# Optimization experiments

Measured on AMD Instinct MI355X. Metric: run time of the kernel, lower is better.

## Reference

```python
import jax, jax.numpy as jnp
import numpy as np
import math

D_MODEL = 256; N_LEVELS = 5; N_HEADS = 8; N_POINTS = 4
D_HEAD = D_MODEL // N_HEADS
BS = 1; T = 5; H = 64; W = 96


def conv3x3(x, w, b):
    # x: (N, C, H, W), w: (O, C, 3, 3) -> SAME padding conv
    y = jax.lax.conv_general_dilated(x, w, (1, 1), ((1, 1), (1, 1)),
                                     dimension_numbers=('NCHW', 'OIHW', 'NCHW'))
    return y + b[None, :, None, None]


def bilinear_zero(img, px, py):
    # img: (C, Hh, Ww); px, py: (...) pixel coords; zero padding outside.
    C, Hh, Ww = img.shape
    x0 = jnp.floor(px); y0 = jnp.floor(py)
    wx1 = px - x0; wx0 = 1.0 - wx1
    wy1 = py - y0; wy0 = 1.0 - wy1

    def gather(xi, yi):
        valid = (xi >= 0) & (xi < Ww) & (yi >= 0) & (yi < Hh)
        xc = jnp.clip(xi, 0, Ww - 1).astype(jnp.int32)
        yc = jnp.clip(yi, 0, Hh - 1).astype(jnp.int32)
        return img[:, yc, xc] * valid.astype(img.dtype)

    return (gather(x0, y0) * (wx0 * wy0) + gather(x0 + 1, y0) * (wx1 * wy0)
            + gather(x0, y0 + 1) * (wx0 * wy1) + gather(x0 + 1, y0 + 1) * (wx1 * wy1))


def warp(x, flo):
    # x: (b, c, h, w), flo: (b, 2, h, w); grid_sample(align_corners=True) equivalent
    b, c, h, w = x.shape
    gy, gx = jnp.meshgrid(jnp.arange(h, dtype=x.dtype), jnp.arange(w, dtype=x.dtype), indexing='ij')
    px = gx[None] + flo[:, 0]
    py = gy[None] + flo[:, 1]
    return jax.vmap(bilinear_zero)(x, px, py)


def flow_guid_offset(ff, fb, offset):
    # ff, fb: (b, 4, 2, h, w); offset: (N, T*h*w, heads, L, P, 2)
    N, THW, heads, L, P, _ = offset.shape
    hw = THW // L
    off = offset.reshape(N, L, hw, heads, L, P, 2)
    f01, f12, f23, f34 = ff[:, 0], ff[:, 1], ff[:, 2], ff[:, 3]
    f02 = f01 + warp(f12, f01)
    f03 = f02 + warp(f23, f02)
    f04 = f03 + warp(f34, f03)
    f13 = f12 + warp(f23, f12)
    f14 = f13 + warp(f34, f13)
    f24 = f23 + warp(f34, f23)
    b10, b21, b32, b43 = fb[:, 0], fb[:, 1], fb[:, 2], fb[:, 3]
    b42 = b43 + warp(b32, b43)
    b41 = b42 + warp(b21, b42)
    b40 = b41 + warp(b10, b41)
    b31 = b32 + warp(b21, b32)
    b30 = b31 + warp(b10, b31)
    b20 = b21 + warp(b10, b21)

    def flat(f):  # (b, 2, h, w) -> (b, hw, 2)
        return f.transpose(0, 2, 3, 1).reshape(f.shape[0], -1, 2)

    z = jnp.zeros_like(flat(f01))
    adds = jnp.stack([
        jnp.stack([z, flat(f01), flat(f02), flat(f03), flat(f04)], axis=2),
        jnp.stack([flat(b10), z, flat(f12), flat(f13), flat(f14)], axis=2),
        jnp.stack([flat(b20), flat(b21), z, flat(f23), flat(f24)], axis=2),
        jnp.stack([flat(b30), flat(b31), flat(b32), z, flat(f34)], axis=2),
        # NOTE: source repeats chunk3's flows for chunk4 (kept faithfully)
        jnp.stack([flat(b30), flat(b31), flat(b32), z, flat(f34)], axis=2),
    ], axis=1)  # (b, L, hw, L, 2)
    off = off + adds[:, :, :, None, :, None, :]
    return off.reshape(N, THW, heads, L, P, 2)


def _forward(query, input_flatten, reference_points, input_spatial_shapes,
             input_level_start_index, input_padding_mask, flow_forward, flow_backward,
             w_off, b_off, w_attn, b_attn, w_val, b_val, w_out, b_out):
    bs, t, c, h, w = query.shape
    q2 = query.reshape(bs * t, c, h, w)
    value = conv3x3(input_flatten.reshape(bs * t, c, h, w), w_val, b_val)
    off = conv3x3(q2, w_off, b_off)      # (bs*t, heads*L*P*2, h, w)
    aw = conv3x3(q2, w_attn, b_attn)     # (bs*t, heads*L*P, h, w)
    Lq = t * h * w

    def to_tokens(x):  # (bs*t, C, h, w) -> (bs, t*h*w, C)
        return x.reshape(bs, t, -1, h * w).transpose(0, 1, 3, 2).reshape(bs, Lq, -1)

    value = to_tokens(value)
    off = to_tokens(off)
    aw = to_tokens(aw)
    value = jnp.where(input_padding_mask[..., None], jnp.zeros((), value.dtype), value)
    value = value.reshape(bs, Lq, N_HEADS, D_HEAD)
    off = off.reshape(bs, Lq, N_HEADS, N_LEVELS, N_POINTS, 2)
    off = flow_guid_offset(flow_forward, flow_backward, off)
    aw = jax.nn.softmax(aw.reshape(bs, Lq, N_HEADS, N_LEVELS * N_POINTS), axis=-1)
    aw = aw.reshape(bs, Lq, N_HEADS, N_LEVELS, N_POINTS)
    # sampling locations, normalized by (W_l, H_l)
    normalizer = jnp.stack([input_spatial_shapes[:, 1], input_spatial_shapes[:, 0]], -1).astype(off.dtype)
    loc = reference_points[:, :, None, :, None, :] + off / normalizer[None, None, None, :, None, :]
    # core: multi-scale deformable bilinear sampling (grid_sample align_corners=False)
    value_lvl = value.reshape(bs, t, h * w, N_HEADS, D_HEAD)
    out = jnp.zeros((bs * N_HEADS, D_HEAD, Lq), dtype=value.dtype)
    for lvl in range(N_LEVELS):
        v = value_lvl[:, lvl].reshape(bs, h, w, N_HEADS, D_HEAD)
        v = v.transpose(0, 3, 4, 1, 2).reshape(bs * N_HEADS, D_HEAD, h, w)
        l = loc[:, :, :, lvl]  # (bs, Lq, heads, P, 2)
        px = (l[..., 0] * w - 0.5).transpose(0, 2, 1, 3).reshape(bs * N_HEADS, Lq, N_POINTS)
        py = (l[..., 1] * h - 0.5).transpose(0, 2, 1, 3).reshape(bs * N_HEADS, Lq, N_POINTS)
        samp = jax.vmap(bilinear_zero)(v, px, py)  # (bs*heads, D_HEAD, Lq, P)
        w_l = aw[:, :, :, lvl].transpose(0, 2, 1, 3).reshape(bs * N_HEADS, 1, Lq, N_POINTS)
        out = out + jnp.sum(samp * w_l, axis=-1)
    out = out.reshape(bs, N_HEADS, D_HEAD, Lq).transpose(0, 3, 1, 2).reshape(bs, Lq, c)
    out = out.reshape(bs, t, h * w, c).transpose(0, 1, 3, 2).reshape(bs * t, c, h, w)
    out = conv3x3(out, w_out, b_out)
    return out.reshape(bs, t, c, h, w)


def setup_inputs() -> dict:
    key = jax.random.key(0)
    ks = jax.random.split(key, 10)
    Lq = T * H * W
    query = jax.random.normal(ks[0], (BS, T, D_MODEL, H, W), jnp.float32)
    input_flatten = jax.random.normal(ks[1], (BS, T, D_MODEL, H, W), jnp.float32)
    reference_points = jax.random.uniform(ks[2], (BS, Lq, N_LEVELS, 2), jnp.float32)
    input_spatial_shapes = jnp.tile(jnp.array([[H, W]], jnp.int32), (N_LEVELS, 1))
    input_level_start_index = jnp.arange(N_LEVELS, dtype=jnp.int32) * (H * W)
    input_padding_mask = jnp.zeros((BS, Lq), dtype=bool)
    flow_forward = jax.random.normal(ks[3], (BS, 4, 2, H, W), jnp.float32) * 2.0
    flow_backward = jax.random.normal(ks[4], (BS, 4, 2, H, W), jnp.float32) * 2.0

    def xavier(k, shape):
        fan_in = shape[1] * shape[2] * shape[3]
        fan_out = shape[0] * shape[2] * shape[3]
        lim = math.sqrt(6.0 / (fan_in + fan_out))
        return jax.random.uniform(k, shape, jnp.float32, -lim, lim)

    w_off = jax.random.normal(ks[5], (N_HEADS * N_LEVELS * N_POINTS * 2, D_MODEL, 3, 3), jnp.float32) * 0.01
    # bias init follows _reset_parameters grid_init
    thetas = np.arange(N_HEADS) * (2.0 * np.pi / N_HEADS)
    grid = np.stack([np.cos(thetas), np.sin(thetas)], -1)
    grid = grid / np.abs(grid).max(-1, keepdims=True)
    grid = np.tile(grid.reshape(N_HEADS, 1, 1, 2), (1, N_LEVELS, N_POINTS, 1))
    for i in range(N_POINTS):
        grid[:, :, i, :] *= i + 1
    b_off = jnp.asarray(grid.reshape(-1), jnp.float32)
    w_attn = jax.random.normal(ks[6], (N_HEADS * N_LEVELS * N_POINTS, D_MODEL, 3, 3), jnp.float32) * 0.01
    b_attn = jnp.zeros((N_HEADS * N_LEVELS * N_POINTS,), jnp.float32)
    w_val = xavier(ks[7], (D_MODEL, D_MODEL, 3, 3)); b_val = jnp.zeros((D_MODEL,), jnp.float32)
    w_out = xavier(ks[8], (D_MODEL, D_MODEL, 3, 3)); b_out = jnp.zeros((D_MODEL,), jnp.float32)
    return {"query": query, "input_flatten": input_flatten, "reference_points": reference_points,
            "input_spatial_shapes": input_spatial_shapes, "input_level_start_index": input_level_start_index,
            "input_padding_mask": input_padding_mask, "flow_forward": flow_forward, "flow_backward": flow_backward,
            "w_off": w_off, "b_off": b_off, "w_attn": w_attn, "b_attn": b_attn,
            "w_val": w_val, "b_val": b_val, "w_out": w_out, "b_out": b_out}


def reference(query, input_flatten, reference_points, input_spatial_shapes,
              input_level_start_index, input_padding_mask, flow_forward, flow_backward,
              w_off, b_off, w_attn, b_attn, w_val, b_val, w_out, b_out):
    return _forward(query, input_flatten, reference_points, input_spatial_shapes,
                    input_level_start_index, input_padding_mask, flow_forward, flow_backward,
                    w_off, b_off, w_attn, b_attn, w_val, b_val, w_out, b_out)
```

## Files before the change

### kernel.cpp

```cpp
#include <hip/hip_runtime.h>
#include <hip/hip_bf16.h>
#include <hip/hip_fp16.h>

typedef __hip_bfloat16 bf16;
typedef __attribute__((ext_vector_type(8))) short short8;
typedef __attribute__((ext_vector_type(4))) float float4v;

#define T_  5
#define H_  64
#define W_  96
#define HW_ (H_*W_)
#define C_  256
#define NH_ 8
#define DH_ 32
#define NL_ 5
#define NP_ 4
#define LQ_ (T_*HW_)
#define UNITS_ (LQ_*NH_)

#define PH_ 66
#define PW_ 98

static __device__ __forceinline__ void gl2lds16(const bf16* g, bf16* l){
  __builtin_amdgcn_global_load_lds(
      (const __attribute__((address_space(1))) unsigned int*)g,
      (__attribute__((address_space(3))) unsigned int*)l, 16, 0, 0);
}

__global__ __launch_bounds__(256) void zfill_k(float4* __restrict__ p, int n4){
  int i = blockIdx.x*256 + threadIdx.x;
  if (i < n4){ float4 z; z.x=z.y=z.z=z.w=0.f; p[i]=z; }
}

__global__ __launch_bounds__(256) void pad_in_k(const float* __restrict__ in0,
                                                const float* __restrict__ in1,
                                                bf16* __restrict__ pad0,
                                                bf16* __restrict__ pad1){
  __shared__ bf16 sb[256][66];
  const float* in = blockIdx.z ? in1 : in0;
  bf16* pad       = blockIdx.z ? pad1 : pad0;
  int t = blockIdx.y;
  int pix0 = blockIdx.x*64;
  int tid = threadIdx.x;
  int pl = tid & 63, cg = tid >> 6;
  #pragma unroll 4
  for (int it=0; it<64; ++it){
    int c = it*4 + cg;
    sb[c][pl] = __float2bfloat16(in[((size_t)t*C_ + c)*HW_ + pix0 + pl]);
  }
  __syncthreads();
  for (int p=0; p<64; ++p){
    int pix = pix0 + p;
    int y = pix/W_, x = pix - y*W_;
    pad[(((size_t)t*PH_ + y+1)*PW_ + x+1)*C_ + tid] = sb[tid][p];
  }
}

#define S0_ 589824
#define S1_ 1179648
__global__ __launch_bounds__(256) void wt_all_k(const float* __restrict__ wv,
                                                const float* __restrict__ wo,
                                                const float* __restrict__ wa,
                                                const float* __restrict__ wout,
                                                const float* __restrict__ bo,
                                                const float* __restrict__ ba,
                                                bf16* __restrict__ WTv,
                                                bf16* __restrict__ WToa,
                                                bf16* __restrict__ WTout,
                                                float* __restrict__ boa){
  int idx = blockIdx.x*256 + threadIdx.x;
  if (idx < S0_){
    int n = idx/2304, r = idx - n*2304; int tap = r>>8, ci = r&255;
    WTv[idx] = __float2bfloat16(wv[((size_t)(n*C_+ci))*9 + tap]);
  } else if (idx < S0_+S1_){
    int k = idx - S0_;
    int n = k/2304, r = k - n*2304; int tap=r>>8, ci=r&255;
    float v = 0.f;
    if (n < 320)      v = wo[((size_t)(n*C_+ci))*9+tap];
    else if (n < 480) v = wa[((size_t)((n-320)*C_+ci))*9+tap];
    WToa[k] = __float2bfloat16(v);
  } else if (idx < S0_+S1_+S0_){
    int k = idx - S0_ - S1_;
    int n = k/2304, r = k - n*2304; int tap=r>>8, ci=r&255;
    WTout[k] = __float2bfloat16(wout[((size_t)(n*C_+ci))*9+tap]);
  } else if (idx < S0_+S1_+S0_+512){
    int n = idx - (S0_+S1_+S0_);
    float v = 0.f;
    if (n < 320) v = bo[n]; else if (n < 480) v = ba[n-320];
    boa[n] = v;
  }
}

#define BM 128
#define BN 256
#define BK 64

__global__ __launch_bounds__(256,2) void gemm12_k(const bf16* __restrict__ Av,
                                                  const bf16* __restrict__ Aq,
                                                  const bf16* __restrict__ WTv,
                                                  const bf16* __restrict__ WToa,
                                                  const float* __restrict__ bv,
                                                  const float* __restrict__ boa,
                                                  bf16* __restrict__ outv,
                                                  float* __restrict__ P,
                                                  float* __restrict__ aw){
  __shared__ __align__(16) bf16 As[BM*BK];
  __shared__ __align__(16) bf16 Bs[BN*BK];
  int tid = threadIdx.x;
  int lane = tid & 63, wvi = tid >> 6;
  int wm = wvi & 1, wn = wvi >> 1;
  int quad = lane >> 4, l15 = lane & 15;
  int bx = blockIdx.x, byy = blockIdx.y;
  bool isval = byy == 0;
  const bf16* Apad  = isval ? Av  : Aq;
  const bf16* WT    = isval ? WTv : WToa;
  const float* bias = isval ? bv  : boa;
  int nby = isval ? 0 : byy - 1;

  int srow = tid >> 3;
  int c8   = (tid & 7) ^ (srow & 7);
  long abase[4];
  #pragma unroll
  for (int j=0;j<4;++j){
    int p = j*32 + srow;
    int Pm = bx*BM + p;
    int t = Pm / HW_, rem = Pm - t*HW_;
    int y = rem / W_, x = rem - y*W_;
    abase[j] = ((long)(t*PH_ + y)*PW_ + x)*C_ + c8*8;
  }
  const bf16* bbase = WT + (size_t)(nby*BN + srow)*2304 + c8*8;

  float4v acc[4][8];
  #pragma unroll
  for (int jn=0;jn<8;++jn){
    float bvv = bias[nby*BN + wn*128 + jn*16 + l15];
    #pragma unroll
    for (int i=0;i<4;++i){ acc[i][jn][0]=bvv; acc[i][jn][1]=bvv; acc[i][jn][2]=bvv; acc[i][jn][3]=bvv; }
  }

  for (int kt=0; kt<36; ++kt){
    int tap = kt >> 2, kc = (kt & 3) << 6;
    int dy = tap/3, dx = tap - dy*3;
    long ash = (long)(dy*PW_ + dx)*C_ + kc;
    long bsh = (long)kt*64;
    __syncthreads();
    #pragma unroll
    for (int j=0;j<4;++j)
      gl2lds16(Apad + abase[j] + ash, As + (j*256+tid)*8);
    #pragma unroll
    for (int j=0;j<8;++j)
      gl2lds16(bbase + (size_t)j*32*2304 + bsh, Bs + (j*256+tid)*8);
    __syncthreads();
    #pragma unroll
    for (int kk=0; kk<2; ++kk){
      int slot = ((kk<<2) + quad) ^ (l15 & 7);
      short8 af[4], bfr[8];
      #pragma unroll
      for (int jn=0;jn<8;++jn)
        bfr[jn] = *(const short8*)(Bs + (wn*128 + jn*16 + l15)*BK + slot*8);
      #pragma unroll
      for (int i=0;i<4;++i)
        af[i] = *(const short8*)(As + (wm*64 + i*16 + l15)*BK + slot*8);
      #pragma unroll
      for (int i=0;i<4;++i)
        #pragma unroll
        for (int jn=0;jn<8;++jn)
          acc[i][jn] = __builtin_amdgcn_mfma_f32_16x16x32_bf16(af[i], bfr[jn], acc[i][jn], 0,0,0);
    }
  }

  #pragma unroll
  for (int i=0;i<4;++i){
    int mr = bx*BM + wm*64 + i*16 + quad*4;
    #pragma unroll
    for (int jn=0;jn<8;++jn){
      int nc = nby*BN + wn*128 + jn*16 + l15;
      #pragma unroll
      for (int r=0;r<4;++r){
        float v = acc[i][jn][r];
        long m = mr + r;
        if (isval){
          outv[m*256 + nc] = __float2bfloat16(v);
        } else {
          if (nc < 320){
            int h = nc/40, rr = nc - h*40;
            int l = rr >> 3, pxy = rr & 7;
            P[((size_t)l*UNITS_ + m*8 + h)*8 + pxy] = v;
          } else if (nc < 480){
            int hh = (nc-320)/20, ii = (nc-320) - hh*20;
            aw[((size_t)m*8 + hh)*20 + ii] = v;
          }
        }
      }
    }
  }
}

__global__ __launch_bounds__(256,2) void gemm_out_k(const bf16* __restrict__ Apad,
                                                    const bf16* __restrict__ WT,
                                                    const float* __restrict__ bias,
                                                    float* __restrict__ out){
  __shared__ __align__(16) bf16 As[BM*BK];
  __shared__ __align__(16) bf16 Bs[BN*BK];
  int tid = threadIdx.x;
  int lane = tid & 63, wvi = tid >> 6;
  int wm = wvi & 1, wn = wvi >> 1;
  int quad = lane >> 4, l15 = lane & 15;
  int bx = blockIdx.x;

  int srow = tid >> 3;
  int c8   = (tid & 7) ^ (srow & 7);
  long abase[4];
  #pragma unroll
  for (int j=0;j<4;++j){
    int p = j*32 + srow;
    int Pm = bx*BM + p;
    int t = Pm / HW_, rem = Pm - t*HW_;
    int y = rem / W_, x = rem - y*W_;
    abase[j] = ((long)(t*PH_ + y)*PW_ + x)*C_ + c8*8;
  }
  const bf16* bbase = WT + (size_t)srow*2304 + c8*8;

  float4v acc[4][8];
  #pragma unroll
  for (int jn=0;jn<8;++jn){
    float bvv = bias[wn*128 + jn*16 + l15];
    #pragma unroll
    for (int i=0;i<4;++i){ acc[i][jn][0]=bvv; acc[i][jn][1]=bvv; acc[i][jn][2]=bvv; acc[i][jn][3]=bvv; }
  }

  for (int kt=0; kt<36; ++kt){
    int tap = kt >> 2, kc = (kt & 3) << 6;
    int dy = tap/3, dx = tap - dy*3;
    long ash = (long)(dy*PW_ + dx)*C_ + kc;
    long bsh = (long)kt*64;
    __syncthreads();
    #pragma unroll
    for (int j=0;j<4;++j)
      gl2lds16(Apad + abase[j] + ash, As + (j*256+tid)*8);
    #pragma unroll
    for (int j=0;j<8;++j)
      gl2lds16(bbase + (size_t)j*32*2304 + bsh, Bs + (j*256+tid)*8);
    __syncthreads();
    #pragma unroll
    for (int kk=0; kk<2; ++kk){
      int slot = ((kk<<2) + quad) ^ (l15 & 7);
      short8 af[4], bfr[8];
      #pragma unroll
      for (int jn=0;jn<8;++jn)
        bfr[jn] = *(const short8*)(Bs + (wn*128 + jn*16 + l15)*BK + slot*8);
      #pragma unroll
      for (int i=0;i<4;++i)
        af[i] = *(const short8*)(As + (wm*64 + i*16 + l15)*BK + slot*8);
      #pragma unroll
      for (int i=0;i<4;++i)
        #pragma unroll
        for (int jn=0;jn<8;++jn)
          acc[i][jn] = __builtin_amdgcn_mfma_f32_16x16x32_bf16(af[i], bfr[jn], acc[i][jn], 0,0,0);
    }
  }

  int t = (bx*BM) / HW_;
  #pragma unroll
  for (int i=0;i<4;++i){
    int m = bx*BM + wm*64 + i*16 + quad*4;
    int pix = m - t*HW_;
    #pragma unroll
    for (int jn=0;jn<8;++jn){
      int nc = wn*128 + jn*16 + l15;
      *(float4v*)(out + ((size_t)(t*C_ + nc))*HW_ + pix) = acc[i][jn];
    }
  }
}

static __device__ __forceinline__ float bilin2(const float* __restrict__ img,
                                               float px, float py){
  float x0f = floorf(px), y0f = floorf(py);
  int x0 = (int)x0f, y0 = (int)y0f;
  float fx = px - x0f, fy = py - y0f;
  int x1 = x0+1, y1 = y0+1;
  bool vx0 = (x0>=0)&&(x0<W_), vx1 = (x1>=0)&&(x1<W_);
  bool vy0 = (y0>=0)&&(y0<H_), vy1 = (y1>=0)&&(y1<H_);
  float c00 = (vx0&&vy0)? img[y0*W_+x0] : 0.f;
  float c10 = (vx1&&vy0)? img[y0*W_+x1] : 0.f;
  float c01 = (vx0&&vy1)? img[y1*W_+x0] : 0.f;
  float c11 = (vx1&&vy1)? img[y1*W_+x1] : 0.f;
  return c00*(1.f-fx)*(1.f-fy) + c10*fx*(1.f-fy) + c01*(1.f-fx)*fy + c11*fx*fy;
}

__global__ __launch_bounds__(256) void flow_init_k(const float* __restrict__ ff,
                                                   const float* __restrict__ fb,
                                                   float* __restrict__ flows){
  int i = blockIdx.x*256 + threadIdx.x;
  const int per = 2*HW_;
  if (i >= 7*per) return;
  int f = i/per, r = i - f*per;
  float v; int slot;
  if (f < 4) { v = ff[f*per + r]; slot = f; }
  else       { v = fb[(f-4)*per + r]; slot = 10+(f-4); }
  flows[slot*per + r] = v;
}

struct Comps { int dst[5]; int a[5]; int src[5]; };

__global__ __launch_bounds__(256) void flow_compose_k(float* __restrict__ flows, Comps c){
  int ci  = blockIdx.y;
  int pix = blockIdx.x*256 + threadIdx.x;
  float* D       = flows + c.dst[ci]*2*HW_;
  const float* A = flows + c.a[ci]  *2*HW_;
  const float* S = flows + c.src[ci]*2*HW_;
  float ax = A[pix], ay = A[HW_+pix];
  float px = (float)(pix % W_) + ax;
  float py = (float)(pix / W_) + ay;
  D[pix]      = ax + bilin2(S,      px, py);
  D[HW_+pix]  = ay + bilin2(S+HW_,  px, py);
}

__device__ const int g_slotTab[25] = {
  -1,  0,  4,  5,  6,
  10, -1,  1,  7,  8,
  13, 11, -1,  2,  9,
  15, 14, 12, -1,  3,
  15, 14, 12, -1,  3 };

__global__ __launch_bounds__(256) void prep_k(const float* __restrict__ aw,
                                              const float* __restrict__ ref,
                                              const float* __restrict__ flows,
                                              float* __restrict__ P,
                                              __half* __restrict__ w16){
  int unit = blockIdx.x*256 + threadIdx.x;
  const float4* p4 = (const float4*)(aw + (size_t)unit*20);
  float4 v[5];
  #pragma unroll
  for (int i=0;i<5;++i) v[i] = p4[i];
  float* e = (float*)v;
  float m = -1e30f;
  #pragma unroll
  for (int i=0;i<20;++i) m = fmaxf(m, e[i]);
  float s = 0.f;
  #pragma unroll
  for (int i=0;i<20;++i){ e[i] = __expf(e[i]-m); s += e[i]; }
  float inv = 1.f/s;
  __half2* o2 = (__half2*)(w16 + (size_t)unit*20);
  #pragma unroll
  for (int i=0;i<10;++i)
    o2[i] = __floats2half2_rn(e[2*i]*inv, e[2*i+1]*inv);

  int q = unit >> 3;
  int t_q = q / HW_, pix = q - t_q*HW_;
  #pragma unroll
  for (int l=0; l<NL_; ++l){
    int slot = g_slotTab[t_q*5+l];
    float ax=0.f, ay=0.f;
    if (slot >= 0){ ax = flows[slot*2*HW_ + pix]; ay = flows[slot*2*HW_ + HW_ + pix]; }
    float bx = ref[(q*5+l)*2+0]*(float)W_ - 0.5f + ax;
    float by = ref[(q*5+l)*2+1]*(float)H_ - 0.5f + ay;
    float2* pp = (float2*)(P + ((size_t)l*UNITS_ + unit)*8);
    #pragma unroll
    for (int p=0;p<4;++p){ float2 t = pp[p]; t.x += bx; t.y += by; pp[p] = t; }
  }
}

template<bool FIRST, bool LAST>
__global__ __launch_bounds__(256) void phase_k(const unsigned* __restrict__ vimg0,
                                               const float2*  __restrict__ Pl,
                                               const __half*  __restrict__ wl,
                                               __half2* __restrict__ acc,
                                               bf16* __restrict__ attn_pad){
  __shared__ float4 sW[16][4];
  __shared__ int4   sI[16][4];
  int tid = threadIdx.x;
  if (tid < 64){
    int g = tid >> 2, p = tid & 3;
    int unit = blockIdx.x*16 + g;
    float2 pp = Pl[(size_t)unit*4 + p];
    float w = __half2float(wl[(size_t)unit*20 + p]);
    float x0f = floorf(pp.x), y0f = floorf(pp.y);
    float fx = pp.x - x0f,    fy = pp.y - y0f;
    int x0 = (int)x0f, y0 = (int)y0f;
    int x1 = x0+1, y1 = y0+1;
    float wx0 = 1.f-fx, wx1 = fx, wy0 = 1.f-fy, wy1 = fy;
    if ((unsigned)x0 >= (unsigned)W_) wx0 = 0.f;
    if ((unsigned)x1 >= (unsigned)W_) wx1 = 0.f;
    if ((unsigned)y0 >= (unsigned)H_) wy0 = 0.f;
    if ((unsigned)y1 >= (unsigned)H_) wy1 = 0.f;
    int xc0 = min(max(x0,0),W_-1), xc1 = min(max(x1,0),W_-1);
    int yc0 = min(max(y0,0),H_-1), yc1 = min(max(y1,0),H_-1);
    sW[g][p] = make_float4(w*wx0*wy0, w*wx1*wy0, w*wx0*wy1, w*wx1*wy1);
    sI[g][p] = make_int4((yc0*W_+xc0)*128, (yc0*W_+xc1)*128,
                         (yc1*W_+xc0)*128, (yc1*W_+xc1)*128);
  }
  __syncthreads();
  int g = tid >> 4, e = tid & 15;
  int unit = blockIdx.x*16 + g;
  int q = unit >> 3, h = unit & 7;
  const unsigned* vimg = vimg0 + h*16 + e;
  float a0, a1;
  if (FIRST){ a0 = 0.f; a1 = 0.f; }
  else { __half2 c = acc[(size_t)unit*16 + e]; a0 = __low2float(c); a1 = __high2float(c); }
  #pragma unroll
  for (int p=0; p<4; ++p){
    float4 w4 = sW[g][p];
    int4   i4 = sI[g][p];
    unsigned u00 = vimg[i4.x], u10 = vimg[i4.y];
    unsigned u01 = vimg[i4.z], u11 = vimg[i4.w];
    union {unsigned v; float f;} lo, hi;
    lo.v = u00<<16; hi.v = u00 & 0xffff0000u;
    a0 = fmaf(w4.x, lo.f, a0); a1 = fmaf(w4.x, hi.f, a1);
    lo.v = u10<<16; hi.v = u10 & 0xffff0000u;
    a0 = fmaf(w4.y, lo.f, a0); a1 = fmaf(w4.y, hi.f, a1);
    lo.v = u01<<16; hi.v = u01 & 0xffff0000u;
    a0 = fmaf(w4.z, lo.f, a0); a1 = fmaf(w4.z, hi.f, a1);
    lo.v = u11<<16; hi.v = u11 & 0xffff0000u;
    a0 = fmaf(w4.w, lo.f, a0); a1 = fmaf(w4.w, hi.f, a1);
  }
  if (LAST){
    int t_q = q / HW_, pix = q - t_q*HW_;
    int yq = pix / W_, xq = pix - yq*W_;
    union {unsigned u; bf16 hh[2];} pk;
    pk.hh[0] = __float2bfloat16(a0);
    pk.hh[1] = __float2bfloat16(a1);
    *(unsigned*)(attn_pad + (((size_t)t_q*PH_ + yq+1)*PW_ + xq+1)*C_ + h*DH_ + e*2) = pk.u;
  } else {
    acc[(size_t)unit*16 + e] = __floats2half2_rn(a0, a1);
  }
}

extern "C" void kernel_launch(void* const* d_in, const int* in_sizes, int n_in,
                              void* d_out, int out_size, void* d_ws, size_t ws_size,
                              hipStream_t stream) {
  const float* query   = (const float*)d_in[0];
  const float* in_flat = (const float*)d_in[1];
  const float* refpts  = (const float*)d_in[2];
  const float* ff      = (const float*)d_in[6];
  const float* fb      = (const float*)d_in[7];
  const float* w_off   = (const float*)d_in[8];
  const float* b_off   = (const float*)d_in[9];
  const float* w_attn  = (const float*)d_in[10];
  const float* b_attn  = (const float*)d_in[11];
  const float* w_val   = (const float*)d_in[12];
  const float* b_val   = (const float*)d_in[13];
  const float* w_out   = (const float*)d_in[14];
  const float* b_out   = (const float*)d_in[15];
  float* out = (float*)d_out;

  char* ws = (char*)d_ws;
  bf16*  v_pad   = (bf16*) (ws + 0);
  bf16*  q_pad   = (bf16*) (ws + 16558080);
  __half* w16    = (__half*)(ws + 16558080);
  bf16*  v_val   = (bf16*) (ws + 33116160);
  float* P       = (float*)(ws + 48844800);
  float* v_aw    = (float*)(ws + 88166400);
  __half2* acc   = (__half2*)(ws + 88166400);
  float* v_flows = (float*)(ws + 107827200);
  bf16*  WT_val  = (bf16*) (ws + 108613632);
  bf16*  WT_oa   = (bf16*) (ws + 109793280);
  bf16*  WT_out  = (bf16*) (ws + 112152576);
  float* bias_oa = (float*)(ws + 113332224);
  bf16*  attn_pad = v_pad;
  if (ws_size < (size_t)113334272) return;

  zfill_k<<<(2069760+255)/256, 256, 0, stream>>>((float4*)v_pad, 2069760);

  wt_all_k<<<(S0_+S1_+S0_+512+255)/256, 256, 0, stream>>>(
      w_val, w_off, w_attn, w_out, b_off, b_attn, WT_val, WT_oa, WT_out, bias_oa);

  flow_init_k<<<(7*2*HW_+255)/256, 256, 0, stream>>>(ff, fb, v_flows);
  Comps A;
  A.dst[0]=4;  A.a[0]=0;  A.src[0]=1;
  A.dst[1]=7;  A.a[1]=1;  A.src[1]=2;
  A.dst[2]=9;  A.a[2]=2;  A.src[2]=3;
  A.dst[3]=13; A.a[3]=11; A.src[3]=10;
  A.dst[4]=14; A.a[4]=12; A.src[4]=11;
  flow_compose_k<<<dim3(HW_/256,5), 256, 0, stream>>>(v_flows, A);
  Comps B;
  B.dst[0]=5;  B.a[0]=4;  B.src[0]=2;
  B.dst[1]=8;  B.a[1]=7;  B.src[1]=3;
  B.dst[2]=15; B.a[2]=14; B.src[2]=10;
  B.dst[3]=0;  B.a[3]=0;  B.src[3]=0;
  B.dst[4]=0;  B.a[4]=0;  B.src[4]=0;
  flow_compose_k<<<dim3(HW_/256,3), 256, 0, stream>>>(v_flows, B);
  Comps Cc;
  Cc.dst[0]=6; Cc.a[0]=5; Cc.src[0]=3;
  Cc.dst[1]=0; Cc.a[1]=0; Cc.src[1]=0;
  Cc.dst[2]=0; Cc.a[2]=0; Cc.src[2]=0;
  Cc.dst[3]=0; Cc.a[3]=0; Cc.src[3]=0;
  Cc.dst[4]=0; Cc.a[4]=0; Cc.src[4]=0;
  flow_compose_k<<<dim3(HW_/256,1), 256, 0, stream>>>(v_flows, Cc);

  pad_in_k<<<dim3(HW_/64, T_, 2), 256, 0, stream>>>(in_flat, query, v_pad, q_pad);

  gemm12_k<<<dim3(240, 3), 256, 0, stream>>>(v_pad, q_pad, WT_val, WT_oa,
                                             b_val, bias_oa, v_val, P, v_aw);

  prep_k<<<UNITS_/256, 256, 0, stream>>>(v_aw, refpts, v_flows, P, w16);

  {
    const unsigned* vb = (const unsigned*)v_val;
    phase_k<true ,false><<<UNITS_/16, 256, 0, stream>>>(vb + 0ul*HW_*128,
        (const float2*)(P + 0ul*UNITS_*8), w16 + 0,  acc, attn_pad);
    phase_k<false,false><<<UNITS_/16, 256, 0, stream>>>(vb + 1ul*HW_*128,
        (const float2*)(P + 1ul*UNITS_*8), w16 + 4,  acc, attn_pad);
    phase_k<false,false><<<UNITS_/16, 256, 0, stream>>>(vb + 2ul*HW_*128,
        (const float2*)(P + 2ul*UNITS_*8), w16 + 8,  acc, attn_pad);
    phase_k<false,false><<<UNITS_/16, 256, 0, stream>>>(vb + 3ul*HW_*128,
        (const float2*)(P + 3ul*UNITS_*8), w16 + 12, acc, attn_pad);
    phase_k<false,true ><<<UNITS_/16, 256, 0, stream>>>(vb + 4ul*HW_*128,
        (const float2*)(P + 4ul*UNITS_*8), w16 + 16, acc, attn_pad);
  }

  gemm_out_k<<<dim3(240, 1), 256, 0, stream>>>(attn_pad, WT_out, b_out, out);
}
```

Baseline: 484.9 us.

## Double-buffer conv GEMM LDS tiles with BK=32 and async prefetch

Both implicit-GEMM conv kernels now use two LDS buffers with a K-step of 32 instead of a single BK=64 buffer. The global-to-LDS loads for the next step are issued before computing the current one, with explicit vmcnt waits and barriers replacing the two __syncthreads per step. MFMA issue priority is raised during compute, and the LDS swizzle is changed to match the narrower tiles. The aim is to hide global load latency behind MFMA work, at the cost of twice as many loop iterations and barriers per K step.

```diff
diff --git a/kernel.cpp b/kernel.cpp
--- a/kernel.cpp
+++ b/kernel.cpp
@@ -93,7 +93,20 @@
 
 #define BM 128
 #define BN 256
-#define BK 64
+#define BKH 32
+
+#define STAGE6(buf, kt_) do {                                              \
+    int tap_ = (kt_) >> 3, kc_ = ((kt_) & 7) << 5;                         \
+    int dy_ = tap_/3, dx_ = tap_ - dy_*3;                                  \
+    long ash_ = (long)(dy_*PW_ + dx_)*C_ + kc_;                            \
+    long bsh_ = (long)tap_*256 + kc_;                                      \
+    gl2lds16(Apad + abase[0] + ash_, &As[buf][(0*256+tid)*8]);             \
+    gl2lds16(Apad + abase[1] + ash_, &As[buf][(1*256+tid)*8]);             \
+    gl2lds16(bbase + 0ul*64*2304 + bsh_, &Bs[buf][(0*256+tid)*8]);         \
+    gl2lds16(bbase + 1ul*64*2304 + bsh_, &Bs[buf][(1*256+tid)*8]);         \
+    gl2lds16(bbase + 2ul*64*2304 + bsh_, &Bs[buf][(2*256+tid)*8]);         \
+    gl2lds16(bbase + 3ul*64*2304 + bsh_, &Bs[buf][(3*256+tid)*8]);         \
+  } while(0)
 
 __global__ __launch_bounds__(256,2) void gemm12_k(const bf16* __restrict__ Av,
                                                   const bf16* __restrict__ Aq,
@@ -104,8 +117,8 @@
                                                   bf16* __restrict__ outv,
                                                   float* __restrict__ P,
                                                   float* __restrict__ aw){
-  __shared__ __align__(16) bf16 As[BM*BK];
-  __shared__ __align__(16) bf16 Bs[BN*BK];
+  __shared__ __align__(16) bf16 As[2][BM*BKH];
+  __shared__ __align__(16) bf16 Bs[2][BN*BKH];
   int tid = threadIdx.x;
   int lane = tid & 63, wvi = tid >> 6;
   int wm = wvi & 1, wn = wvi >> 1;
@@ -117,18 +130,18 @@
   const float* bias = isval ? bv  : boa;
   int nby = isval ? 0 : byy - 1;
 
-  int srow = tid >> 3;
-  int c8   = (tid & 7) ^ (srow & 7);
-  long abase[4];
-  #pragma unroll
-  for (int j=0;j<4;++j){
-    int p = j*32 + srow;
+  int sr = tid >> 2;
+  int sc = (tid & 3) ^ ((tid >> 3) & 3);
+  long abase[2];
+  #pragma unroll
+  for (int it=0; it<2; ++it){
+    int p = it*64 + sr;
     int Pm = bx*BM + p;
     int t = Pm / HW_, rem = Pm - t*HW_;
     int y = rem / W_, x = rem - y*W_;
-    abase[j] = ((long)(t*PH_ + y)*PW_ + x)*C_ + c8*8;
-  }
-  const bf16* bbase = WT + (size_t)(nby*BN + srow)*2304 + c8*8;
+    abase[it] = ((long)(t*PH_ + y)*PW_ + x)*C_ + sc*8;
+  }
+  const bf16* bbase = WT + (size_t)(nby*BN + sr)*2304 + sc*8;
 
   float4v acc[4][8];
   #pragma unroll
@@ -137,36 +150,41 @@
     #pragma unroll
     for (int i=0;i<4;++i){ acc[i][jn][0]=bvv; acc[i][jn][1]=bvv; acc[i][jn][2]=bvv; acc[i][jn][3]=bvv; }
   }
-
-  for (int kt=0; kt<36; ++kt){
-    int tap = kt >> 2, kc = (kt & 3) << 6;
-    int dy = tap/3, dx = tap - dy*3;
-    long ash = (long)(dy*PW_ + dx)*C_ + kc;
-    long bsh = (long)kt*64;
-    __syncthreads();
-    #pragma unroll
-    for (int j=0;j<4;++j)
-      gl2lds16(Apad + abase[j] + ash, As + (j*256+tid)*8);
-    #pragma unroll
-    for (int j=0;j<8;++j)
-      gl2lds16(bbase + (size_t)j*32*2304 + bsh, Bs + (j*256+tid)*8);
-    __syncthreads();
-    #pragma unroll
-    for (int kk=0; kk<2; ++kk){
-      int slot = ((kk<<2) + quad) ^ (l15 & 7);
-      short8 af[4], bfr[8];
+  asm volatile("s_waitcnt vmcnt(0)" ::: "memory");
+  __builtin_amdgcn_sched_barrier(0);
+
+  STAGE6(0, 0);
+  int sxor = (l15 >> 1) & 3;
+  for (int kt=0; kt<72; ++kt){
+    int cur = kt & 1;
+    if (kt < 71){
+      STAGE6(cur^1, kt+1);
+      asm volatile("s_waitcnt vmcnt(6)" ::: "memory");
+    } else {
+      asm volatile("s_waitcnt vmcnt(0)" ::: "memory");
+    }
+    __builtin_amdgcn_sched_barrier(0);
+    __builtin_amdgcn_s_barrier();
+    __builtin_amdgcn_sched_barrier(0);
+    int gq = quad ^ sxor;
+    short8 af[4], bfr[8];
+    #pragma unroll
+    for (int jn=0;jn<8;++jn)
+      bfr[jn] = *(const short8*)(&Bs[cur][(wn*128 + jn*16 + l15)*BKH + gq*8]);
+    #pragma unroll
+    for (int i=0;i<4;++i)
+      af[i] = *(const short8*)(&As[cur][(wm*64 + i*16 + l15)*BKH + gq*8]);
+    __builtin_amdgcn_s_setprio(1);
+    #pragma unroll
+    for (int i=0;i<4;++i)
       #pragma unroll
       for (int jn=0;jn<8;++jn)
-        bfr[jn] = *(const short8*)(Bs + (wn*128 + jn*16 + l15)*BK + slot*8);
-      #pragma unroll
-      for (int i=0;i<4;++i)
-        af[i] = *(const short8*)(As + (wm*64 + i*16 + l15)*BK + slot*8);
-      #pragma unroll
-      for (int i=0;i<4;++i)
-        #pragma unroll
-        for (int jn=0;jn<8;++jn)
-          acc[i][jn] = __builtin_amdgcn_mfma_f32_16x16x32_bf16(af[i], bfr[jn], acc[i][jn], 0,0,0);
-    }
+        acc[i][jn] = __builtin_amdgcn_mfma_f32_16x16x32_bf16(af[i], bfr[jn], acc[i][jn], 0,0,0);
+    __builtin_amdgcn_s_setprio(0);
+    asm volatile("s_waitcnt lgkmcnt(0)" ::: "memory");
+    __builtin_amdgcn_sched_barrier(0);
+    __builtin_amdgcn_s_barrier();
+    __builtin_amdgcn_sched_barrier(0);
   }
 
   #pragma unroll
@@ -200,26 +218,26 @@
                                                     const bf16* __restrict__ WT,
                                                     const float* __restrict__ bias,
                                                     float* __restrict__ out){
-  __shared__ __align__(16) bf16 As[BM*BK];
-  __shared__ __align__(16) bf16 Bs[BN*BK];
+  __shared__ __align__(16) bf16 As[2][BM*BKH];
+  __shared__ __align__(16) bf16 Bs[2][BN*BKH];
   int tid = threadIdx.x;
   int lane = tid & 63, wvi = tid >> 6;
   int wm = wvi & 1, wn = wvi >> 1;
   int quad = lane >> 4, l15 = lane & 15;
   int bx = blockIdx.x;
 
-  int srow = tid >> 3;
-  int c8   = (tid & 7) ^ (srow & 7);
-  long abase[4];
-  #pragma unroll
-  for (int j=0;j<4;++j){
-    int p = j*32 + srow;
+  int sr = tid >> 2;
+  int sc = (tid & 3) ^ ((tid >> 3) & 3);
+  long abase[2];
+  #pragma unroll
+  for (int it=0; it<2; ++it){
+    int p = it*64 + sr;
     int Pm = bx*BM + p;
     int t = Pm / HW_, rem = Pm - t*HW_;
     int y = rem / W_, x = rem - y*W_;
-    abase[j] = ((long)(t*PH_ + y)*PW_ + x)*C_ + c8*8;
-  }
-  const bf16* bbase = WT + (size_t)srow*2304 + c8*8;
+    abase[it] = ((long)(t*PH_ + y)*PW_ + x)*C_ + sc*8;
+  }
+  const bf16* bbase = WT + (size_t)sr*2304 + sc*8;
 
   float4v acc[4][8];
   #pragma unroll
@@ -228,36 +246,41 @@
     #pragma unroll
     for (int i=0;i<4;++i){ acc[i][jn][0]=bvv; acc[i][jn][1]=bvv; acc[i][jn][2]=bvv; acc[i][jn][3]=bvv; }
   }
-
-  for (int kt=0; kt<36; ++kt){
-    int tap = kt >> 2, kc = (kt & 3) << 6;
-    int dy = tap/3, dx = tap - dy*3;
-    long ash = (long)(dy*PW_ + dx)*C_ + kc;
-    long bsh = (long)kt*64;
-    __syncthreads();
-    #pragma unroll
-    for (int j=0;j<4;++j)
-      gl2lds16(Apad + abase[j] + ash, As + (j*256+tid)*8);
-    #pragma unroll
-    for (int j=0;j<8;++j)
-      gl2lds16(bbase + (size_t)j*32*2304 + bsh, Bs + (j*256+tid)*8);
-    __syncthreads();
-    #pragma unroll
-    for (int kk=0; kk<2; ++kk){
-      int slot = ((kk<<2) + quad) ^ (l15 & 7);
-      short8 af[4], bfr[8];
+  asm volatile("s_waitcnt vmcnt(0)" ::: "memory");
+  __builtin_amdgcn_sched_barrier(0);
+
+  STAGE6(0, 0);
+  int sxor = (l15 >> 1) & 3;
+  for (int kt=0; kt<72; ++kt){
+    int cur = kt & 1;
+    if (kt < 71){
+      STAGE6(cur^1, kt+1);
+      asm volatile("s_waitcnt vmcnt(6)" ::: "memory");
+    } else {
+      asm volatile("s_waitcnt vmcnt(0)" ::: "memory");
+    }
+    __builtin_amdgcn_sched_barrier(0);
+    __builtin_amdgcn_s_barrier();
+    __builtin_amdgcn_sched_barrier(0);
+    int gq = quad ^ sxor;
+    short8 af[4], bfr[8];
+    #pragma unroll
+    for (int jn=0;jn<8;++jn)
+      bfr[jn] = *(const short8*)(&Bs[cur][(wn*128 + jn*16 + l15)*BKH + gq*8]);
+    #pragma unroll
+    for (int i=0;i<4;++i)
+      af[i] = *(const short8*)(&As[cur][(wm*64 + i*16 + l15)*BKH + gq*8]);
+    __builtin_amdgcn_s_setprio(1);
+    #pragma unroll
+    for (int i=0;i<4;++i)
       #pragma unroll
       for (int jn=0;jn<8;++jn)
-        bfr[jn] = *(const short8*)(Bs + (wn*128 + jn*16 + l15)*BK + slot*8);
-      #pragma unroll
-      for (int i=0;i<4;++i)
-        af[i] = *(const short8*)(As + (wm*64 + i*16 + l15)*BK + slot*8);
-      #pragma unroll
-      for (int i=0;i<4;++i)
-        #pragma unroll
-        for (int jn=0;jn<8;++jn)
-          acc[i][jn] = __builtin_amdgcn_mfma_f32_16x16x32_bf16(af[i], bfr[jn], acc[i][jn], 0,0,0);
-    }
+        acc[i][jn] = __builtin_amdgcn_mfma_f32_16x16x32_bf16(af[i], bfr[jn], acc[i][jn], 0,0,0);
+    __builtin_amdgcn_s_setprio(0);
+    asm volatile("s_waitcnt lgkmcnt(0)" ::: "memory");
+    __builtin_amdgcn_sched_barrier(0);
+    __builtin_amdgcn_s_barrier();
+    __builtin_amdgcn_sched_barrier(0);
   }
 
   int t = (bx*BM) / HW_;
```

New measurement: 523.3 us. 1.08x slower.

## Fuse softmax prep and five per-level sampling kernels into one kernel

Applied to the files above, without the earlier changes.

Replaces prep_k and five per-level phase_k launches with a single phases_k that computes softmax weights, sampling locations and bilinear weights for all levels in shared memory, then accumulates all levels in registers. This removes the global read-modify-write of P, the fp16 weight buffer, and the fp16 accumulator round trips between levels. It trades per-level cache locality of value images for a larger working set per block and more shared memory.

```diff
diff --git a/kernel.cpp b/kernel.cpp
--- a/kernel.cpp
+++ b/kernel.cpp
@@ -323,60 +323,50 @@
   15, 14, 12, -1,  3,
   15, 14, 12, -1,  3 };
 
-__global__ __launch_bounds__(256) void prep_k(const float* __restrict__ aw,
-                                              const float* __restrict__ ref,
-                                              const float* __restrict__ flows,
-                                              float* __restrict__ P,
-                                              __half* __restrict__ w16){
-  int unit = blockIdx.x*256 + threadIdx.x;
-  const float4* p4 = (const float4*)(aw + (size_t)unit*20);
-  float4 v[5];
-  #pragma unroll
-  for (int i=0;i<5;++i) v[i] = p4[i];
-  float* e = (float*)v;
-  float m = -1e30f;
-  #pragma unroll
-  for (int i=0;i<20;++i) m = fmaxf(m, e[i]);
-  float s = 0.f;
-  #pragma unroll
-  for (int i=0;i<20;++i){ e[i] = __expf(e[i]-m); s += e[i]; }
-  float inv = 1.f/s;
-  __half2* o2 = (__half2*)(w16 + (size_t)unit*20);
-  #pragma unroll
-  for (int i=0;i<10;++i)
-    o2[i] = __floats2half2_rn(e[2*i]*inv, e[2*i+1]*inv);
-
-  int q = unit >> 3;
-  int t_q = q / HW_, pix = q - t_q*HW_;
-  #pragma unroll
-  for (int l=0; l<NL_; ++l){
+__global__ __launch_bounds__(256) void phases_k(const unsigned* __restrict__ vb,
+                                                const float*   __restrict__ P,
+                                                const float*   __restrict__ aw,
+                                                const float*   __restrict__ ref,
+                                                const float*   __restrict__ flows,
+                                                bf16* __restrict__ attn_pad){
+  __shared__ float4 sW[5][16][4];
+  __shared__ int4   sI[5][16][4];
+  __shared__ float  sE[16][20];
+  __shared__ float  sM[16], sR[16];
+  int tid = threadIdx.x;
+  int unit0 = blockIdx.x*16;
+
+  for (int s = tid; s < 320; s += 256){
+    int l = s >> 6, r = s & 63;
+    int g = r >> 2, p = r & 3;
+    sE[g][l*4+p] = aw[(size_t)(unit0+g)*20 + l*4 + p];
+  }
+  __syncthreads();
+  if (tid < 16){
+    float m = -1e30f;
+    #pragma unroll
+    for (int i=0;i<20;++i) m = fmaxf(m, sE[tid][i]);
+    float ssum = 0.f;
+    #pragma unroll
+    for (int i=0;i<20;++i) ssum += __expf(sE[tid][i]-m);
+    sM[tid] = m; sR[tid] = 1.f/ssum;
+  }
+  __syncthreads();
+  for (int s = tid; s < 320; s += 256){
+    int l = s >> 6, r = s & 63;
+    int g = r >> 2, p = r & 3;
+    int unit = unit0 + g;
+    float w = __expf(sE[g][l*4+p] - sM[g]) * sR[g];
+    int q = unit >> 3;
+    int t_q = q / HW_, pix = q - t_q*HW_;
     int slot = g_slotTab[t_q*5+l];
-    float ax=0.f, ay=0.f;
+    float ax = 0.f, ay = 0.f;
     if (slot >= 0){ ax = flows[slot*2*HW_ + pix]; ay = flows[slot*2*HW_ + HW_ + pix]; }
-    float bx = ref[(q*5+l)*2+0]*(float)W_ - 0.5f + ax;
-    float by = ref[(q*5+l)*2+1]*(float)H_ - 0.5f + ay;
-    float2* pp = (float2*)(P + ((size_t)l*UNITS_ + unit)*8);
-    #pragma unroll
-    for (int p=0;p<4;++p){ float2 t = pp[p]; t.x += bx; t.y += by; pp[p] = t; }
-  }
-}
-
-template<bool FIRST, bool LAST>
-__global__ __launch_bounds__(256) void phase_k(const unsigned* __restrict__ vimg0,
-                                               const float2*  __restrict__ Pl,
-                                               const __half*  __restrict__ wl,
-                                               __half2* __restrict__ acc,
-                                               bf16* __restrict__ attn_pad){
-  __shared__ float4 sW[16][4];
-  __shared__ int4   sI[16][4];
-  int tid = threadIdx.x;
-  if (tid < 64){
-    int g = tid >> 2, p = tid & 3;
-    int unit = blockIdx.x*16 + g;
-    float2 pp = Pl[(size_t)unit*4 + p];
-    float w = __half2float(wl[(size_t)unit*20 + p]);
-    float x0f = floorf(pp.x), y0f = floorf(pp.y);
-    float fx = pp.x - x0f,    fy = pp.y - y0f;
+    float2 pr = ((const float2*)P)[((size_t)l*UNITS_ + unit)*4 + p];
+    float px = pr.x + ref[(q*5+l)*2+0]*(float)W_ - 0.5f + ax;
+    float py = pr.y + ref[(q*5+l)*2+1]*(float)H_ - 0.5f + ay;
+    float x0f = floorf(px), y0f = floorf(py);
+    float fx = px - x0f,    fy = py - y0f;
     int x0 = (int)x0f, y0 = (int)y0f;
     int x1 = x0+1, y1 = y0+1;
     float wx0 = 1.f-fx, wx1 = fx, wy0 = 1.f-fy, wy1 = fy;
@@ -386,44 +376,41 @@
     if ((unsigned)y1 >= (unsigned)H_) wy1 = 0.f;
     int xc0 = min(max(x0,0),W_-1), xc1 = min(max(x1,0),W_-1);
     int yc0 = min(max(y0,0),H_-1), yc1 = min(max(y1,0),H_-1);
-    sW[g][p] = make_float4(w*wx0*wy0, w*wx1*wy0, w*wx0*wy1, w*wx1*wy1);
-    sI[g][p] = make_int4((yc0*W_+xc0)*128, (yc0*W_+xc1)*128,
-                         (yc1*W_+xc0)*128, (yc1*W_+xc1)*128);
+    sW[l][g][p] = make_float4(w*wx0*wy0, w*wx1*wy0, w*wx0*wy1, w*wx1*wy1);
+    sI[l][g][p] = make_int4((yc0*W_+xc0)*128, (yc0*W_+xc1)*128,
+                            (yc1*W_+xc0)*128, (yc1*W_+xc1)*128);
   }
   __syncthreads();
   int g = tid >> 4, e = tid & 15;
-  int unit = blockIdx.x*16 + g;
+  int unit = unit0 + g;
   int q = unit >> 3, h = unit & 7;
-  const unsigned* vimg = vimg0 + h*16 + e;
-  float a0, a1;
-  if (FIRST){ a0 = 0.f; a1 = 0.f; }
-  else { __half2 c = acc[(size_t)unit*16 + e]; a0 = __low2float(c); a1 = __high2float(c); }
-  #pragma unroll
-  for (int p=0; p<4; ++p){
-    float4 w4 = sW[g][p];
-    int4   i4 = sI[g][p];
-    unsigned u00 = vimg[i4.x], u10 = vimg[i4.y];
-    unsigned u01 = vimg[i4.z], u11 = vimg[i4.w];
-    union {unsigned v; float f;} lo, hi;
-    lo.v = u00<<16; hi.v = u00 & 0xffff0000u;
-    a0 = fmaf(w4.x, lo.f, a0); a1 = fmaf(w4.x, hi.f, a1);
-    lo.v = u10<<16; hi.v = u10 & 0xffff0000u;
-    a0 = fmaf(w4.y, lo.f, a0); a1 = fmaf(w4.y, hi.f, a1);
-    lo.v = u01<<16; hi.v = u01 & 0xffff0000u;
-    a0 = fmaf(w4.z, lo.f, a0); a1 = fmaf(w4.z, hi.f, a1);
-    lo.v = u11<<16; hi.v = u11 & 0xffff0000u;
-    a0 = fmaf(w4.w, lo.f, a0); a1 = fmaf(w4.w, hi.f, a1);
-  }
-  if (LAST){
-    int t_q = q / HW_, pix = q - t_q*HW_;
-    int yq = pix / W_, xq = pix - yq*W_;
-    union {unsigned u; bf16 hh[2];} pk;
-    pk.hh[0] = __float2bfloat16(a0);
-    pk.hh[1] = __float2bfloat16(a1);
-    *(unsigned*)(attn_pad + (((size_t)t_q*PH_ + yq+1)*PW_ + xq+1)*C_ + h*DH_ + e*2) = pk.u;
-  } else {
-    acc[(size_t)unit*16 + e] = __floats2half2_rn(a0, a1);
-  }
+  float a0 = 0.f, a1 = 0.f;
+  #pragma unroll
+  for (int l=0; l<5; ++l){
+    const unsigned* vimg = vb + (size_t)l*HW_*128 + h*16 + e;
+    #pragma unroll
+    for (int p=0; p<4; ++p){
+      float4 w4 = sW[l][g][p];
+      int4   i4 = sI[l][g][p];
+      unsigned u00 = vimg[i4.x], u10 = vimg[i4.y];
+      unsigned u01 = vimg[i4.z], u11 = vimg[i4.w];
+      union {unsigned v; float f;} lo, hi;
+      lo.v = u00<<16; hi.v = u00 & 0xffff0000u;
+      a0 = fmaf(w4.x, lo.f, a0); a1 = fmaf(w4.x, hi.f, a1);
+      lo.v = u10<<16; hi.v = u10 & 0xffff0000u;
+      a0 = fmaf(w4.y, lo.f, a0); a1 = fmaf(w4.y, hi.f, a1);
+      lo.v = u01<<16; hi.v = u01 & 0xffff0000u;
+      a0 = fmaf(w4.z, lo.f, a0); a1 = fmaf(w4.z, hi.f, a1);
+      lo.v = u11<<16; hi.v = u11 & 0xffff0000u;
+      a0 = fmaf(w4.w, lo.f, a0); a1 = fmaf(w4.w, hi.f, a1);
+    }
+  }
+  int t_q = q / HW_, pix = q - t_q*HW_;
+  int yq = pix / W_, xq = pix - yq*W_;
+  union {unsigned u; bf16 hh[2];} pk;
+  pk.hh[0] = __float2bfloat16(a0);
+  pk.hh[1] = __float2bfloat16(a1);
+  *(unsigned*)(attn_pad + (((size_t)t_q*PH_ + yq+1)*PW_ + xq+1)*C_ + h*DH_ + e*2) = pk.u;
 }
 
 extern "C" void kernel_launch(void* const* d_in, const int* in_sizes, int n_in,
@@ -447,11 +434,9 @@
   char* ws = (char*)d_ws;
   bf16*  v_pad   = (bf16*) (ws + 0);
   bf16*  q_pad   = (bf16*) (ws + 16558080);
-  __half* w16    = (__half*)(ws + 16558080);
   bf16*  v_val   = (bf16*) (ws + 33116160);
   float* P       = (float*)(ws + 48844800);
   float* v_aw    = (float*)(ws + 88166400);
-  __half2* acc   = (__half2*)(ws + 88166400);
   float* v_flows = (float*)(ws + 107827200);
   bf16*  WT_val  = (bf16*) (ws + 108613632);
   bf16*  WT_oa   = (bf16*) (ws + 109793280);
@@ -493,21 +478,8 @@
   gemm12_k<<<dim3(240, 3), 256, 0, stream>>>(v_pad, q_pad, WT_val, WT_oa,
                                              b_val, bias_oa, v_val, P, v_aw);
 
-  prep_k<<<UNITS_/256, 256, 0, stream>>>(v_aw, refpts, v_flows, P, w16);
-
-  {
-    const unsigned* vb = (const unsigned*)v_val;
-    phase_k<true ,false><<<UNITS_/16, 256, 0, stream>>>(vb + 0ul*HW_*128,
-        (const float2*)(P + 0ul*UNITS_*8), w16 + 0,  acc, attn_pad);
-    phase_k<false,false><<<UNITS_/16, 256, 0, stream>>>(vb + 1ul*HW_*128,
-        (const float2*)(P + 1ul*UNITS_*8), w16 + 4,  acc, attn_pad);
-    phase_k<false,false><<<UNITS_/16, 256, 0, stream>>>(vb + 2ul*HW_*128,
-        (const float2*)(P + 2ul*UNITS_*8), w16 + 8,  acc, attn_pad);
-    phase_k<false,false><<<UNITS_/16, 256, 0, stream>>>(vb + 3ul*HW_*128,
-        (const float2*)(P + 3ul*UNITS_*8), w16 + 12, acc, attn_pad);
-    phase_k<false,true ><<<UNITS_/16, 256, 0, stream>>>(vb + 4ul*HW_*128,
-        (const float2*)(P + 4ul*UNITS_*8), w16 + 16, acc, attn_pad);
-  }
+  phases_k<<<UNITS_/16, 256, 0, stream>>>((const unsigned*)v_val, P, v_aw,
+                                          refpts, v_flows, attn_pad);
 
   gemm_out_k<<<dim3(240, 1), 256, 0, stream>>>(attn_pad, WT_out, b_out, out);
 }
```

New measurement: 530.6 us. 1.09x slower.
